# Kernel tuning notes

Measured on AMD Instinct MI355X. Metric: run time of the kernel, lower is better.

The kernel has to match this reference:

```python
import jax, jax.numpy as jnp
import numpy as np

N_NODES = 50000
N_EDGES = 800000
IN_DIM = 96
HID = 96


def setup_inputs() -> dict:
    key = jax.random.key(0)
    k1, k2, k3, k4 = jax.random.split(key, 4)
    x = jax.random.normal(k1, (N_NODES, IN_DIM), dtype=jnp.float32)
    edge_index = jax.random.randint(k2, (2, N_EDGES), 0, N_NODES, dtype=jnp.int64)
    s1 = 1.0 / np.sqrt(IN_DIM)
    s2 = 1.0 / np.sqrt(HID)
    W1 = jax.random.normal(k3, (IN_DIM, HID), dtype=jnp.float32) * s1
    b1 = jnp.zeros((HID,), dtype=jnp.float32)
    W2 = jax.random.normal(k4, (HID, HID), dtype=jnp.float32) * s2
    b2 = jnp.zeros((HID,), dtype=jnp.float32)
    return {"x": x, "edge_index": edge_index, "W1": W1, "b1": b1, "W2": W2, "b2": b2}


def _gcn_conv(x, src, dst, norm, W, b, n_nodes):
    # x' = D^{-1/2}(A+I)D^{-1/2} X W + b  (PyG GCNConv semantics)
    xw = x @ W                           # [N, out]
    msg = xw[src] * norm[:, None]        # gather + edge-normalize, [E+N, out]
    agg = jax.ops.segment_sum(msg, dst, num_segments=n_nodes)  # scatter-add
    return agg + b


def reference(x, edge_index, W1, b1, W2, b2):
    n_nodes = x.shape[0]
    loops = jnp.arange(n_nodes, dtype=edge_index.dtype)
    src = jnp.concatenate([edge_index[0], loops])  # sources (j)
    dst = jnp.concatenate([edge_index[1], loops])  # targets (i), aggregation index
    # symmetric normalization with self-loops; degree counted at targets
    deg = jax.ops.segment_sum(jnp.ones(dst.shape, dtype=x.dtype), dst, num_segments=n_nodes)
    dinv = jnp.where(deg > 0, jax.lax.rsqrt(deg), 0.0)
    norm = dinv[src] * dinv[dst]
    h = jax.nn.relu(_gcn_conv(x, src, dst, norm, W1, b1, n_nodes))
    h = jax.nn.relu(_gcn_conv(h, src, dst, norm, W2, b2, n_nodes))
    return h
```

## Files before the change

### kernel.cpp

```cpp
#include <hip/hip_runtime.h>

#define N_NODES 50000
#define N_EDGES 800000
#define DIM 96
#define FEAT_ELEMS (N_NODES * DIM)
#define NBLK 196

typedef __attribute__((ext_vector_type(8))) short short8;
typedef __attribute__((ext_vector_type(4))) float float4v;

__device__ __forceinline__ float bf16_to_f32(unsigned short u) {
    unsigned int w = ((unsigned int)u) << 16;
    float f;
    __builtin_memcpy(&f, &w, 4);
    return f;
}
__device__ __forceinline__ unsigned short f32_to_bf16_rne(float f) {
    unsigned int w;
    __builtin_memcpy(&w, &f, 4);
    unsigned int r = (w + 0x7FFFu + ((w >> 16) & 1u)) >> 16;
    return (unsigned short)r;
}

__device__ __forceinline__ int edge_at(const void* ep, int is64, int idx) {
    if (is64) return (int)((const long long*)ep)[idx];
    return ((const int*)ep)[idx];
}

__global__ __launch_bounds__(256) void prolog_kernel(const unsigned int* edges,
                                                     const unsigned int* x,
                                                     int* flagE, int* flagF, int* cnt) {
    __shared__ unsigned int sh[256];
    int t = threadIdx.x;
    int b = blockIdx.x;
    if (b < NBLK) {
        int i = b * 256 + t;
        if (i < N_NODES) cnt[i] = 0;
        return;
    }
    if (b == NBLK) {
        if (t < 64) {
            unsigned int acc = 0;
            for (int k = 0; k < 4; ++k) {
                int idx = t * 4 + k;
                int pos = 1 + 2 * idx * 3109;
                acc |= edges[pos];
            }
            sh[t] = acc;
        }
        __syncthreads();
        if (t == 0) {
            unsigned int a = 0;
            for (int i = 0; i < 64; ++i) a |= sh[i];
            *flagE = (a == 0u) ? 1 : 0;
        }
        return;
    }
    unsigned int w = x[t * 9000];
    unsigned int e = (w >> 7) & 0xFFu;
    sh[t] = (e >= 100u && e <= 135u) ? 1u : 0u;
    __syncthreads();
    if (t == 0) {
        int c = 0;
        for (int i = 0; i < 256; ++i) c += (int)sh[i];
        *flagF = (c >= 128) ? 1 : 0;
    }
}

__global__ __launch_bounds__(256) void count_compact_kernel(const void* edges,
                                                            const int* flagE, int* cnt,
                                                            unsigned short* srcu,
                                                            unsigned short* dstu,
                                                            unsigned short* rank) {
    int e = blockIdx.x * 256 + threadIdx.x;
    if (e >= N_EDGES) return;
    int is64 = *flagE;
    int s = edge_at(edges, is64, e);
    int d = edge_at(edges, is64, N_EDGES + e);
    srcu[e] = (unsigned short)s;
    dstu[e] = (unsigned short)d;
    rank[e] = (unsigned short)atomicAdd(&cnt[d], 1);
}

__global__ __launch_bounds__(256) void scan_blocksum_kernel(const int* cnt, int* blockSums) {
    __shared__ int sh[256];
    int i = blockIdx.x * 256 + threadIdx.x;
    sh[threadIdx.x] = (i < N_NODES) ? cnt[i] : 0;
    __syncthreads();
    for (int off = 128; off > 0; off >>= 1) {
        if (threadIdx.x < off) sh[threadIdx.x] += sh[threadIdx.x + off];
        __syncthreads();
    }
    if (threadIdx.x == 0) blockSums[blockIdx.x] = sh[0];
}

__global__ __launch_bounds__(256) void scan_offsets_kernel(const int* blockSums,
                                                           int* blockOffs, int* row_ptr) {
    __shared__ int sh[256];
    int t = threadIdx.x;
    int v = (t < NBLK) ? blockSums[t] : 0;
    sh[t] = v;
    __syncthreads();
    for (int off = 1; off < 256; off <<= 1) {
        int u = (t >= off) ? sh[t - off] : 0;
        __syncthreads();
        sh[t] += u;
        __syncthreads();
    }
    if (t < NBLK) blockOffs[t] = sh[t] - v;
    if (t == 255) row_ptr[N_NODES] = sh[255];
}

__global__ __launch_bounds__(256) void scan_apply_kernel(const int* cnt, const int* blockOffs,
                                                         int* row_ptr, float* dinv) {
    __shared__ int sh[256];
    int t = threadIdx.x;
    int i = blockIdx.x * 256 + t;
    int c = (i < N_NODES) ? cnt[i] : 0;
    sh[t] = c;
    __syncthreads();
    for (int off = 1; off < 256; off <<= 1) {
        int u = (t >= off) ? sh[t - off] : 0;
        __syncthreads();
        sh[t] += u;
        __syncthreads();
    }
    if (i < N_NODES) {
        int excl = sh[t] - c + blockOffs[blockIdx.x];
        row_ptr[i] = excl;
        dinv[i]    = rsqrtf((float)(c + 1));
    }
}

__global__ __launch_bounds__(256) void fill_direct_kernel(const unsigned short* __restrict__ dstu,
                                                          const unsigned short* __restrict__ srcu,
                                                          const unsigned short* __restrict__ rank,
                                                          const int* __restrict__ row_ptr,
                                                          unsigned short* __restrict__ csr_src) {
    int e = blockIdx.x * 256 + threadIdx.x;
    if (e >= N_EDGES) return;
    int d = dstu[e];
    int pos = row_ptr[d] + (int)rank[e];
    csr_src[pos] = srcu[e];
}

__global__ __launch_bounds__(256) void convert_kernel(const void* x, const int* flagF,
                                                      unsigned short* xb) {
    int i4 = (blockIdx.x * 256 + threadIdx.x) * 4;
    if (i4 >= FEAT_ELEMS) return;
    int isbf16 = *flagF;
    ushort4 o;
    if (isbf16) {
        o = *(const ushort4*)((const unsigned short*)x + i4);
    } else {
        float4 v = *(const float4*)((const float*)x + i4);
        o.x = f32_to_bf16_rne(v.x);
        o.y = f32_to_bf16_rne(v.y);
        o.z = f32_to_bf16_rne(v.z);
        o.w = f32_to_bf16_rne(v.w);
    }
    *(ushort4*)(xb + i4) = o;
}

__global__ __launch_bounds__(256) void gather_kernel(const unsigned short* __restrict__ feat,
                                                     const int* __restrict__ row_ptr,
                                                     const unsigned short* __restrict__ csr_src,
                                                     const float* __restrict__ dinv,
                                                     unsigned short* __restrict__ aggb) {
    int gid = blockIdx.x * 256 + threadIdx.x;
    int g = gid >> 4;
    int lane = gid & 15;
    if (g >= N_NODES) return;
    float di = dinv[g];
    int o4 = lane * 4;
    int o2 = 64 + lane * 2;
    int gbase = g * DIM;
    ushort4 sv = *(const ushort4*)&feat[gbase + o4];
    ushort2 sw = *(const ushort2*)&feat[gbase + o2];
    float wself = di * di;
    float a0 = wself * bf16_to_f32(sv.x), a1 = wself * bf16_to_f32(sv.y);
    float a2 = wself * bf16_to_f32(sv.z), a3 = wself * bf16_to_f32(sv.w);
    float a4 = wself * bf16_to_f32(sw.x), a5 = wself * bf16_to_f32(sw.y);
    int e = row_ptr[g], e1 = row_ptr[g + 1];
    for (; e + 2 <= e1; e += 2) {
        int s0 = csr_src[e];
        int s1 = csr_src[e + 1];
        float w0 = dinv[s0] * di;
        float w1 = dinv[s1] * di;
        int b0 = s0 * DIM;
        int b1 = s1 * DIM;
        ushort4 p = *(const ushort4*)&feat[b0 + o4];
        ushort2 pw = *(const ushort2*)&feat[b0 + o2];
        ushort4 q = *(const ushort4*)&feat[b1 + o4];
        ushort2 qw = *(const ushort2*)&feat[b1 + o2];
        a0 = fmaf(w0, bf16_to_f32(p.x), a0);  a1 = fmaf(w0, bf16_to_f32(p.y), a1);
        a2 = fmaf(w0, bf16_to_f32(p.z), a2);  a3 = fmaf(w0, bf16_to_f32(p.w), a3);
        a4 = fmaf(w0, bf16_to_f32(pw.x), a4); a5 = fmaf(w0, bf16_to_f32(pw.y), a5);
        a0 = fmaf(w1, bf16_to_f32(q.x), a0);  a1 = fmaf(w1, bf16_to_f32(q.y), a1);
        a2 = fmaf(w1, bf16_to_f32(q.z), a2);  a3 = fmaf(w1, bf16_to_f32(q.w), a3);
        a4 = fmaf(w1, bf16_to_f32(qw.x), a4); a5 = fmaf(w1, bf16_to_f32(qw.y), a5);
    }
    if (e < e1) {
        int s = csr_src[e];
        float w = dinv[s] * di;
        int b0 = s * DIM;
        ushort4 p = *(const ushort4*)&feat[b0 + o4];
        ushort2 pw = *(const ushort2*)&feat[b0 + o2];
        a0 = fmaf(w, bf16_to_f32(p.x), a0);  a1 = fmaf(w, bf16_to_f32(p.y), a1);
        a2 = fmaf(w, bf16_to_f32(p.z), a2);  a3 = fmaf(w, bf16_to_f32(p.w), a3);
        a4 = fmaf(w, bf16_to_f32(pw.x), a4); a5 = fmaf(w, bf16_to_f32(pw.y), a5);
    }
    uint2 ov;
    ov.x = (unsigned int)f32_to_bf16_rne(a0) | ((unsigned int)f32_to_bf16_rne(a1) << 16);
    ov.y = (unsigned int)f32_to_bf16_rne(a2) | ((unsigned int)f32_to_bf16_rne(a3) << 16);
    unsigned int ow = (unsigned int)f32_to_bf16_rne(a4) | ((unsigned int)f32_to_bf16_rne(a5) << 16);
    *(uint2*)&aggb[gbase + o4] = ov;
    *(unsigned int*)&aggb[gbase + o2] = ow;
}

__global__ __launch_bounds__(256) void gemm_mfma_kernel(const unsigned short* __restrict__ A,
                                                        const void* W, const void* bias,
                                                        const int* flagF,
                                                        void* out, int outMode) {
    __shared__ unsigned short Wlin[DIM * DIM];
    __shared__ unsigned short Wsw[3 * 6 * 64 * 8];
    __shared__ float bs[DIM];
    int wBf16 = *flagF;
    int outBf16 = (outMode == 2) ? wBf16 : outMode;

    if (wBf16) {
        const ushort4* W4 = (const ushort4*)W;
        ushort4* L4 = (ushort4*)Wlin;
        for (int i = threadIdx.x; i < DIM * DIM / 4; i += 256) L4[i] = W4[i];
        if (threadIdx.x < DIM)
            bs[threadIdx.x] = bf16_to_f32(((const unsigned short*)bias)[threadIdx.x]);
    } else {
        const float* Wf = (const float*)W;
        for (int i = threadIdx.x; i < DIM * DIM; i += 256) Wlin[i] = f32_to_bf16_rne(Wf[i]);
        if (threadIdx.x < DIM) bs[threadIdx.x] = ((const float*)bias)[threadIdx.x];
    }
    __syncthreads();

    for (int f = threadIdx.x; f < 1152; f += 256) {
        int kt = f / 384;
        int rem = f - kt * 384;
        int nt = rem >> 6;
        int ln64 = rem & 63;
        int q = ln64 >> 4, ln = ln64 & 15;
        int k0 = kt * 32 + q * 8;
        int n = nt * 16 + ln;
        unsigned int w0 = (unsigned int)Wlin[(k0 + 0) * DIM + n] |
                          ((unsigned int)Wlin[(k0 + 1) * DIM + n] << 16);
        unsigned int w1 = (unsigned int)Wlin[(k0 + 2) * DIM + n] |
                          ((unsigned int)Wlin[(k0 + 3) * DIM + n] << 16);
        unsigned int w2 = (unsigned int)Wlin[(k0 + 4) * DIM + n] |
                          ((unsigned int)Wlin[(k0 + 5) * DIM + n] << 16);
        unsigned int w3 = (unsigned int)Wlin[(k0 + 6) * DIM + n] |
                          ((unsigned int)Wlin[(k0 + 7) * DIM + n] << 16);
        uint4 pk = make_uint4(w0, w1, w2, w3);
        *(uint4*)&Wsw[f * 8] = pk;
    }
    __syncthreads();

    int wave = threadIdx.x >> 6;
    int lane = threadIdx.x & 63;
    int quad = lane >> 4, ln = lane & 15;
    int m0 = blockIdx.x * 64 + wave * 16;
    int arow = m0 + ln;
    bool arowok = (arow < N_NODES);

    float4v acc[6];
    #pragma unroll
    for (int nt = 0; nt < 6; ++nt) acc[nt] = (float4v){0.f, 0.f, 0.f, 0.f};

    #pragma unroll
    for (int kt = 0; kt < 3; ++kt) {
        short8 af;
        if (arowok) {
            af = *(const short8*)&A[arow * DIM + kt * 32 + quad * 8];
        } else {
            af = (short8){0, 0, 0, 0, 0, 0, 0, 0};
        }
        #pragma unroll
        for (int nt = 0; nt < 6; ++nt) {
            short8 bf = *(const short8*)&Wsw[((kt * 6 + nt) * 64 + lane) * 8];
            acc[nt] = __builtin_amdgcn_mfma_f32_16x16x32_bf16(af, bf, acc[nt], 0, 0, 0);
        }
    }

    #pragma unroll
    for (int nt = 0; nt < 6; ++nt) {
        int n = nt * 16 + ln;
        float bv = bs[n];
        #pragma unroll
        for (int reg = 0; reg < 4; ++reg) {
            int row = m0 + quad * 4 + reg;
            if (row >= N_NODES) continue;
            float v = fmaxf(acc[nt][reg] + bv, 0.0f);
            if (outBf16) ((unsigned short*)out)[row * DIM + n] = f32_to_bf16_rne(v);
            else         ((float*)out)[row * DIM + n] = v;
        }
    }
}

extern "C" void kernel_launch(void* const* d_in, const int* in_sizes, int n_in,
                              void* d_out, int out_size, void* d_ws, size_t ws_size,
                              hipStream_t stream) {
    const void* x  = d_in[0];
    const void* ei = d_in[1];
    const void* W1 = d_in[2];
    const void* b1 = d_in[3];
    const void* W2 = d_in[4];
    const void* b2 = d_in[5];

    char* base = (char*)d_ws;
    size_t off = 0;
    auto carve = [&](size_t bytes) -> void* {
        void* p = base + off;
        off += (bytes + 255) & ~(size_t)255;
        return p;
    };
    int*            flagE     = (int*)carve(4);
    int*            flagF     = (int*)carve(4);
    int*            cnt       = (int*)carve((size_t)N_NODES * 4);
    int*            row_ptr   = (int*)carve((size_t)(N_NODES + 1) * 4);
    float*          dinv      = (float*)carve((size_t)N_NODES * 4);
    int*            blockSums = (int*)carve((size_t)NBLK * 4);
    int*            blockOffs = (int*)carve((size_t)NBLK * 4);
    unsigned short* srcu      = (unsigned short*)carve((size_t)N_EDGES * 2);
    unsigned short* dstu      = (unsigned short*)carve((size_t)N_EDGES * 2);
    unsigned short* rank      = (unsigned short*)carve((size_t)N_EDGES * 2);
    unsigned short* csr_src   = (unsigned short*)carve((size_t)N_EDGES * 2);
    unsigned short* aggb      = (unsigned short*)carve((size_t)FEAT_ELEMS * 2);
    unsigned short* xb        = (unsigned short*)carve((size_t)FEAT_ELEMS * 2);
    unsigned short* h         = (unsigned short*)carve((size_t)FEAT_ELEMS * 2);

    const int egrid = (N_EDGES + 255) / 256;
    const int cgrid = (FEAT_ELEMS / 4 + 255) / 256;
    const int agrid = (N_NODES * 16 + 255) / 256;
    const int ggrid = (N_NODES + 63) / 64;

    prolog_kernel<<<NBLK + 2, 256, 0, stream>>>((const unsigned int*)ei,
                                                (const unsigned int*)x, flagE, flagF, cnt);
    count_compact_kernel<<<egrid, 256, 0, stream>>>(ei, flagE, cnt, srcu, dstu, rank);
    scan_blocksum_kernel<<<NBLK, 256, 0, stream>>>(cnt, blockSums);
    scan_offsets_kernel<<<1, 256, 0, stream>>>(blockSums, blockOffs, row_ptr);
    scan_apply_kernel<<<NBLK, 256, 0, stream>>>(cnt, blockOffs, row_ptr, dinv);
    fill_direct_kernel<<<egrid, 256, 0, stream>>>(dstu, srcu, rank, row_ptr, csr_src);
    convert_kernel<<<cgrid, 256, 0, stream>>>(x, flagF, xb);

    gather_kernel<<<agrid, 256, 0, stream>>>(xb, row_ptr, csr_src, dinv, aggb);
    gemm_mfma_kernel<<<ggrid, 256, 0, stream>>>(aggb, W1, b1, flagF, h, 1);

    gather_kernel<<<agrid, 256, 0, stream>>>(h, row_ptr, csr_src, dinv, aggb);
    gemm_mfma_kernel<<<ggrid, 256, 0, stream>>>(aggb, W2, b2, flagF, d_out, 2);
}
```

Baseline: 215.1 us.

## Fuse neighbor gather into MFMA GEMM kernel via shared-memory tile

Merges the per-layer gather kernel and the MFMA GEMM kernel into one. Each 256-thread block aggregates 64 nodes into a padded shared-memory tile that reuses the weight staging buffer, then runs the MFMA GEMM straight from LDS. This drops the global write and re-read of the aggregated feature matrix and one launch per layer. In exchange, each block processes 4 nodes per 16-thread group serially, and the weight swizzle runs before the latency-bound gather, so occupancy and latency hiding in the gather phase may suffer.

```diff
diff --git a/kernel.cpp b/kernel.cpp
--- a/kernel.cpp
+++ b/kernel.cpp
@@ -5,6 +5,8 @@
 #define DIM 96
 #define FEAT_ELEMS (N_NODES * DIM)
 #define NBLK 196
+#define TILE 64
+#define AGG_STRIDE 104
 
 typedef __attribute__((ext_vector_type(8))) short short8;
 typedef __attribute__((ext_vector_type(4))) float float4v;
@@ -162,81 +164,29 @@
     *(ushort4*)(xb + i4) = o;
 }
 
-__global__ __launch_bounds__(256) void gather_kernel(const unsigned short* __restrict__ feat,
-                                                     const int* __restrict__ row_ptr,
-                                                     const unsigned short* __restrict__ csr_src,
-                                                     const float* __restrict__ dinv,
-                                                     unsigned short* __restrict__ aggb) {
-    int gid = blockIdx.x * 256 + threadIdx.x;
-    int g = gid >> 4;
-    int lane = gid & 15;
-    if (g >= N_NODES) return;
-    float di = dinv[g];
-    int o4 = lane * 4;
-    int o2 = 64 + lane * 2;
-    int gbase = g * DIM;
-    ushort4 sv = *(const ushort4*)&feat[gbase + o4];
-    ushort2 sw = *(const ushort2*)&feat[gbase + o2];
-    float wself = di * di;
-    float a0 = wself * bf16_to_f32(sv.x), a1 = wself * bf16_to_f32(sv.y);
-    float a2 = wself * bf16_to_f32(sv.z), a3 = wself * bf16_to_f32(sv.w);
-    float a4 = wself * bf16_to_f32(sw.x), a5 = wself * bf16_to_f32(sw.y);
-    int e = row_ptr[g], e1 = row_ptr[g + 1];
-    for (; e + 2 <= e1; e += 2) {
-        int s0 = csr_src[e];
-        int s1 = csr_src[e + 1];
-        float w0 = dinv[s0] * di;
-        float w1 = dinv[s1] * di;
-        int b0 = s0 * DIM;
-        int b1 = s1 * DIM;
-        ushort4 p = *(const ushort4*)&feat[b0 + o4];
-        ushort2 pw = *(const ushort2*)&feat[b0 + o2];
-        ushort4 q = *(const ushort4*)&feat[b1 + o4];
-        ushort2 qw = *(const ushort2*)&feat[b1 + o2];
-        a0 = fmaf(w0, bf16_to_f32(p.x), a0);  a1 = fmaf(w0, bf16_to_f32(p.y), a1);
-        a2 = fmaf(w0, bf16_to_f32(p.z), a2);  a3 = fmaf(w0, bf16_to_f32(p.w), a3);
-        a4 = fmaf(w0, bf16_to_f32(pw.x), a4); a5 = fmaf(w0, bf16_to_f32(pw.y), a5);
-        a0 = fmaf(w1, bf16_to_f32(q.x), a0);  a1 = fmaf(w1, bf16_to_f32(q.y), a1);
-        a2 = fmaf(w1, bf16_to_f32(q.z), a2);  a3 = fmaf(w1, bf16_to_f32(q.w), a3);
-        a4 = fmaf(w1, bf16_to_f32(qw.x), a4); a5 = fmaf(w1, bf16_to_f32(qw.y), a5);
-    }
-    if (e < e1) {
-        int s = csr_src[e];
-        float w = dinv[s] * di;
-        int b0 = s * DIM;
-        ushort4 p = *(const ushort4*)&feat[b0 + o4];
-        ushort2 pw = *(const ushort2*)&feat[b0 + o2];
-        a0 = fmaf(w, bf16_to_f32(p.x), a0);  a1 = fmaf(w, bf16_to_f32(p.y), a1);
-        a2 = fmaf(w, bf16_to_f32(p.z), a2);  a3 = fmaf(w, bf16_to_f32(p.w), a3);
-        a4 = fmaf(w, bf16_to_f32(pw.x), a4); a5 = fmaf(w, bf16_to_f32(pw.y), a5);
-    }
-    uint2 ov;
-    ov.x = (unsigned int)f32_to_bf16_rne(a0) | ((unsigned int)f32_to_bf16_rne(a1) << 16);
-    ov.y = (unsigned int)f32_to_bf16_rne(a2) | ((unsigned int)f32_to_bf16_rne(a3) << 16);
-    unsigned int ow = (unsigned int)f32_to_bf16_rne(a4) | ((unsigned int)f32_to_bf16_rne(a5) << 16);
-    *(uint2*)&aggb[gbase + o4] = ov;
-    *(unsigned int*)&aggb[gbase + o2] = ow;
-}
-
-__global__ __launch_bounds__(256) void gemm_mfma_kernel(const unsigned short* __restrict__ A,
-                                                        const void* W, const void* bias,
-                                                        const int* flagF,
-                                                        void* out, int outMode) {
-    __shared__ unsigned short Wlin[DIM * DIM];
-    __shared__ unsigned short Wsw[3 * 6 * 64 * 8];
+__global__ __launch_bounds__(256) void fused_layer_kernel(
+        const unsigned short* __restrict__ feat,
+        const int* __restrict__ row_ptr,
+        const unsigned short* __restrict__ csr_src,
+        const float* __restrict__ dinv,
+        const void* W, const void* bias, const int* flagF,
+        void* out, int outMode) {
+    __shared__ __align__(16) unsigned short unionA[DIM * DIM];
+    __shared__ __align__(16) unsigned short Wsw[1152 * 8];
     __shared__ float bs[DIM];
+
     int wBf16 = *flagF;
     int outBf16 = (outMode == 2) ? wBf16 : outMode;
 
     if (wBf16) {
         const ushort4* W4 = (const ushort4*)W;
-        ushort4* L4 = (ushort4*)Wlin;
+        ushort4* L4 = (ushort4*)unionA;
         for (int i = threadIdx.x; i < DIM * DIM / 4; i += 256) L4[i] = W4[i];
         if (threadIdx.x < DIM)
             bs[threadIdx.x] = bf16_to_f32(((const unsigned short*)bias)[threadIdx.x]);
     } else {
         const float* Wf = (const float*)W;
-        for (int i = threadIdx.x; i < DIM * DIM; i += 256) Wlin[i] = f32_to_bf16_rne(Wf[i]);
+        for (int i = threadIdx.x; i < DIM * DIM; i += 256) unionA[i] = f32_to_bf16_rne(Wf[i]);
         if (threadIdx.x < DIM) bs[threadIdx.x] = ((const float*)bias)[threadIdx.x];
     }
     __syncthreads();
@@ -249,25 +199,84 @@
         int q = ln64 >> 4, ln = ln64 & 15;
         int k0 = kt * 32 + q * 8;
         int n = nt * 16 + ln;
-        unsigned int w0 = (unsigned int)Wlin[(k0 + 0) * DIM + n] |
-                          ((unsigned int)Wlin[(k0 + 1) * DIM + n] << 16);
-        unsigned int w1 = (unsigned int)Wlin[(k0 + 2) * DIM + n] |
-                          ((unsigned int)Wlin[(k0 + 3) * DIM + n] << 16);
-        unsigned int w2 = (unsigned int)Wlin[(k0 + 4) * DIM + n] |
-                          ((unsigned int)Wlin[(k0 + 5) * DIM + n] << 16);
-        unsigned int w3 = (unsigned int)Wlin[(k0 + 6) * DIM + n] |
-                          ((unsigned int)Wlin[(k0 + 7) * DIM + n] << 16);
+        unsigned int w0 = (unsigned int)unionA[(k0 + 0) * DIM + n] |
+                          ((unsigned int)unionA[(k0 + 1) * DIM + n] << 16);
+        unsigned int w1 = (unsigned int)unionA[(k0 + 2) * DIM + n] |
+                          ((unsigned int)unionA[(k0 + 3) * DIM + n] << 16);
+        unsigned int w2 = (unsigned int)unionA[(k0 + 4) * DIM + n] |
+                          ((unsigned int)unionA[(k0 + 5) * DIM + n] << 16);
+        unsigned int w3 = (unsigned int)unionA[(k0 + 6) * DIM + n] |
+                          ((unsigned int)unionA[(k0 + 7) * DIM + n] << 16);
         uint4 pk = make_uint4(w0, w1, w2, w3);
         *(uint4*)&Wsw[f * 8] = pk;
+    }
+    __syncthreads();
+
+    unsigned short* aggT = unionA;
+    {
+        int grp = threadIdx.x >> 4;
+        int ln = threadIdx.x & 15;
+        int o4 = ln * 4;
+        int o2 = 64 + ln * 2;
+        #pragma unroll
+        for (int i = 0; i < 4; ++i) {
+            int nl = grp + 16 * i;
+            int g = blockIdx.x * TILE + nl;
+            if (g >= N_NODES) continue;
+            float di = dinv[g];
+            int gbase = g * DIM;
+            ushort4 sv = *(const ushort4*)&feat[gbase + o4];
+            ushort2 sw = *(const ushort2*)&feat[gbase + o2];
+            float wself = di * di;
+            float a0 = wself * bf16_to_f32(sv.x), a1 = wself * bf16_to_f32(sv.y);
+            float a2 = wself * bf16_to_f32(sv.z), a3 = wself * bf16_to_f32(sv.w);
+            float a4 = wself * bf16_to_f32(sw.x), a5 = wself * bf16_to_f32(sw.y);
+            int e = row_ptr[g], e1 = row_ptr[g + 1];
+            for (; e + 2 <= e1; e += 2) {
+                int s0 = csr_src[e];
+                int s1 = csr_src[e + 1];
+                float w0 = dinv[s0] * di;
+                float w1 = dinv[s1] * di;
+                int b0 = s0 * DIM;
+                int b1 = s1 * DIM;
+                ushort4 p = *(const ushort4*)&feat[b0 + o4];
+                ushort2 pw = *(const ushort2*)&feat[b0 + o2];
+                ushort4 q = *(const ushort4*)&feat[b1 + o4];
+                ushort2 qw = *(const ushort2*)&feat[b1 + o2];
+                a0 = fmaf(w0, bf16_to_f32(p.x), a0);  a1 = fmaf(w0, bf16_to_f32(p.y), a1);
+                a2 = fmaf(w0, bf16_to_f32(p.z), a2);  a3 = fmaf(w0, bf16_to_f32(p.w), a3);
+                a4 = fmaf(w0, bf16_to_f32(pw.x), a4); a5 = fmaf(w0, bf16_to_f32(pw.y), a5);
+                a0 = fmaf(w1, bf16_to_f32(q.x), a0);  a1 = fmaf(w1, bf16_to_f32(q.y), a1);
+                a2 = fmaf(w1, bf16_to_f32(q.z), a2);  a3 = fmaf(w1, bf16_to_f32(q.w), a3);
+                a4 = fmaf(w1, bf16_to_f32(qw.x), a4); a5 = fmaf(w1, bf16_to_f32(qw.y), a5);
+            }
+            if (e < e1) {
+                int s = csr_src[e];
+                float w = dinv[s] * di;
+                int b0 = s * DIM;
+                ushort4 p = *(const ushort4*)&feat[b0 + o4];
+                ushort2 pw = *(const ushort2*)&feat[b0 + o2];
+                a0 = fmaf(w, bf16_to_f32(p.x), a0);  a1 = fmaf(w, bf16_to_f32(p.y), a1);
+                a2 = fmaf(w, bf16_to_f32(p.z), a2);  a3 = fmaf(w, bf16_to_f32(p.w), a3);
+                a4 = fmaf(w, bf16_to_f32(pw.x), a4); a5 = fmaf(w, bf16_to_f32(pw.y), a5);
+            }
+            uint2 ov;
+            ov.x = (unsigned int)f32_to_bf16_rne(a0) | ((unsigned int)f32_to_bf16_rne(a1) << 16);
+            ov.y = (unsigned int)f32_to_bf16_rne(a2) | ((unsigned int)f32_to_bf16_rne(a3) << 16);
+            unsigned int ow = (unsigned int)f32_to_bf16_rne(a4) |
+                              ((unsigned int)f32_to_bf16_rne(a5) << 16);
+            int lb = nl * AGG_STRIDE;
+            *(uint2*)&aggT[lb + o4] = ov;
+            *(unsigned int*)&aggT[lb + o2] = ow;
+        }
     }
     __syncthreads();
 
     int wave = threadIdx.x >> 6;
     int lane = threadIdx.x & 63;
     int quad = lane >> 4, ln = lane & 15;
-    int m0 = blockIdx.x * 64 + wave * 16;
-    int arow = m0 + ln;
-    bool arowok = (arow < N_NODES);
+    int m0 = blockIdx.x * TILE + wave * 16;
+    int mloc = wave * 16 + ln;
 
     float4v acc[6];
     #pragma unroll
@@ -275,12 +284,7 @@
 
     #pragma unroll
     for (int kt = 0; kt < 3; ++kt) {
-        short8 af;
-        if (arowok) {
-            af = *(const short8*)&A[arow * DIM + kt * 32 + quad * 8];
-        } else {
-            af = (short8){0, 0, 0, 0, 0, 0, 0, 0};
-        }
+        short8 af = *(const short8*)&aggT[mloc * AGG_STRIDE + kt * 32 + quad * 8];
         #pragma unroll
         for (int nt = 0; nt < 6; ++nt) {
             short8 bf = *(const short8*)&Wsw[((kt * 6 + nt) * 64 + lane) * 8];
@@ -331,14 +335,12 @@
     unsigned short* dstu      = (unsigned short*)carve((size_t)N_EDGES * 2);
     unsigned short* rank      = (unsigned short*)carve((size_t)N_EDGES * 2);
     unsigned short* csr_src   = (unsigned short*)carve((size_t)N_EDGES * 2);
-    unsigned short* aggb      = (unsigned short*)carve((size_t)FEAT_ELEMS * 2);
     unsigned short* xb        = (unsigned short*)carve((size_t)FEAT_ELEMS * 2);
     unsigned short* h         = (unsigned short*)carve((size_t)FEAT_ELEMS * 2);
 
     const int egrid = (N_EDGES + 255) / 256;
     const int cgrid = (FEAT_ELEMS / 4 + 255) / 256;
-    const int agrid = (N_NODES * 16 + 255) / 256;
-    const int ggrid = (N_NODES + 63) / 64;
+    const int fgrid = (N_NODES + TILE - 1) / TILE;
 
     prolog_kernel<<<NBLK + 2, 256, 0, stream>>>((const unsigned int*)ei,
                                                 (const unsigned int*)x, flagE, flagF, cnt);
@@ -349,9 +351,8 @@
     fill_direct_kernel<<<egrid, 256, 0, stream>>>(dstu, srcu, rank, row_ptr, csr_src);
     convert_kernel<<<cgrid, 256, 0, stream>>>(x, flagF, xb);
 
-    gather_kernel<<<agrid, 256, 0, stream>>>(xb, row_ptr, csr_src, dinv, aggb);
-    gemm_mfma_kernel<<<ggrid, 256, 0, stream>>>(aggb, W1, b1, flagF, h, 1);
-
-    gather_kernel<<<agrid, 256, 0, stream>>>(h, row_ptr, csr_src, dinv, aggb);
-    gemm_mfma_kernel<<<ggrid, 256, 0, stream>>>(aggb, W2, b2, flagF, d_out, 2);
-}
+    fused_layer_kernel<<<fgrid, 256, 0, stream>>>(xb, row_ptr, csr_src, dinv,
+                                                  W1, b1, flagF, h, 1);
+    fused_layer_kernel<<<fgrid, 256, 0, stream>>>(h, row_ptr, csr_src, dinv,
+                                                  W2, b2, flagF, d_out, 2);
+}
```

New measurement: 232.4 us. 1.08x slower.
